# Kernel optimization log

Hardware: AMD Instinct MI355X
Metric: run time of the kernel (lower is better)

Reference implementation:

```python
import jax, jax.numpy as jnp
import numpy as np

N = 100_000   # atoms
B = 10_000    # building blocks
E = 320_000   # edges (bb <- atom)
D = 256       # embed_dim
H = 8         # heads
HD = D // H   # head_dim = 32
DIST = 64     # gaussian dist embed dim
MAX_R = 10.0


def setup_inputs() -> dict:
    key = jax.random.key(0)
    ks = jax.random.split(key, 10)
    atom_feats = jax.random.normal(ks[0], (N, D), jnp.float32)
    coords = jax.random.normal(ks[1], (N, 3), jnp.float32) * 3.0
    bb_vec = jnp.sort(jax.random.randint(ks[2], (N,), 0, B, jnp.int32))
    src = jax.random.randint(ks[3], (E,), 0, N, jnp.int32)
    tgt = jax.random.randint(ks[4], (E,), 0, B, jnp.int32)
    # linear params, [in, out] layout (x @ W + b)
    Wq = jax.random.normal(ks[5], (D, D), jnp.float32) / np.sqrt(D)
    Wk = jax.random.normal(ks[6], (D + DIST, D), jnp.float32) / np.sqrt(D + DIST)
    Wv = jax.random.normal(ks[7], (D + DIST, D), jnp.float32) / np.sqrt(D + DIST)
    Wo = jax.random.normal(ks[8], (D, D), jnp.float32) / np.sqrt(D)
    bq = jnp.zeros((D,), jnp.float32)
    bk = jnp.zeros((D,), jnp.float32)
    bv = jnp.zeros((D,), jnp.float32)
    bo = jnp.zeros((D,), jnp.float32)
    return dict(atom_feats=atom_feats, coords=coords, Wq=Wq, bq=bq, Wk=Wk, bk=bk,
                Wv=Wv, bv=bv, Wo=Wo, bo=bo, bb_vec=bb_vec, src=src, tgt=tgt)


def _gaussian_smearing(dist):
    offsets = jnp.linspace(0.0, MAX_R, DIST)            # [DIST]
    coeff = -0.5 / (offsets[1] - offsets[0]) ** 2
    return jnp.exp(coeff * (dist[:, None] - offsets) ** 2)  # [E, DIST]


def reference(atom_feats, coords, Wq, bq, Wk, bk, Wv, bv, Wo, bo, bb_vec, src, tgt):
    # building-block centers: mean coords, summed feats per bb
    counts = jax.ops.segment_sum(jnp.ones((N,), coords.dtype), bb_vec, num_segments=B)
    bb_center_pos = jax.ops.segment_sum(coords, bb_vec, num_segments=B)
    bb_center_pos = bb_center_pos / jnp.maximum(counts, 1.0)[:, None]       # [B, 3]
    bb_center_feats = jax.ops.segment_sum(atom_feats, bb_vec, num_segments=B)  # [B, D]

    # per-edge distance embedding
    edge_vec = coords[src] - bb_center_pos[tgt]                             # [E, 3]
    dist = jnp.sqrt(jnp.sum(edge_vec * edge_vec, axis=-1))                  # [E]
    edge_dist_embed = _gaussian_smearing(dist)                              # [E, DIST]

    # QKV
    q = (bb_center_feats @ Wq + bq).reshape(B, H, HD)                       # [B, H, HD]
    atom_input = jnp.concatenate([atom_feats[src], edge_dist_embed], -1)    # [E, D+DIST]
    k = (atom_input @ Wk + bk).reshape(E, H, HD)
    v = (atom_input @ Wv + bv).reshape(E, H, HD)

    # per-edge attention logits + segment softmax over tgt
    attn = jnp.einsum('ehc,ehc->eh', q[tgt], k) / np.sqrt(HD)               # [E, H]
    seg_max = jax.ops.segment_max(attn, tgt, num_segments=B)                # [B, H]
    ex = jnp.exp(attn - seg_max[tgt])
    denom = jax.ops.segment_sum(ex, tgt, num_segments=B)                    # [B, H]
    attn = ex / (denom[tgt] + 1e-16)

    # weighted scatter-sum of messages
    msg = attn[..., None] * v                                               # [E, H, HD]
    out = jax.ops.segment_sum(msg, tgt, num_segments=B).reshape(B, D)       # [B, D]
    return out @ Wo + bo
```

## Files before the change

### kernel.cpp

```cpp
#include <hip/hip_runtime.h>
#include <math.h>

#define N_ATOMS 100000
#define B_BB    10000
#define E_EDGES 320000
#define D_DIM   256
#define NHEAD   8
#define NDIST   64
#define EPAD    128

#define DELTA   (10.0f/63.0f)
#define GCOEFF  (-0.5f/(DELTA*DELTA))
#define QKSCALE 0.17677669529663687f

__global__ void k_offsets(const int* __restrict__ bb_vec, int* __restrict__ atom_off,
                          int* __restrict__ edge_cnt) {
  int b = blockIdx.x * 256 + threadIdx.x;
  if (b <= B_BB) {
    int lo = 0, hi = N_ATOMS;
    while (lo < hi) { int mid = (lo + hi) >> 1; if (bb_vec[mid] < b) lo = mid + 1; else hi = mid; }
    atom_off[b] = lo;
  }
  if (b < B_BB) edge_cnt[b] = 0;
}

__global__ __launch_bounds__(256) void k_bb_centers(
    const float* __restrict__ af, const float* __restrict__ coords,
    const int* __restrict__ atom_off, float* __restrict__ bbF, float* __restrict__ bb_pos) {
  int t = threadIdx.x;
  for (int b = blockIdx.x; b < B_BB; b += gridDim.x) {
    int s = atom_off[b], e = atom_off[b + 1];
    float acc = 0.f;
    for (int a = s; a < e; a++) acc += af[(size_t)a * D_DIM + t];
    bbF[(size_t)b * D_DIM + t] = acc;
    if (t < 3) {
      float c = 0.f;
      for (int a = s; a < e; a++) c += coords[(size_t)a * 3 + t];
      float cnt = (float)(e - s);
      bb_pos[b * 4 + t] = c / fmaxf(cnt, 1.0f);
    }
  }
}

__global__ __launch_bounds__(256) void k_gemm256(
    const float* __restrict__ A, const float* __restrict__ W,
    const float* __restrict__ bias, float* __restrict__ C, int M) {
  __shared__ __align__(16) float As[16][68];
  __shared__ __align__(16) float Ws[16][64];
  int tid = threadIdx.x;
  int tx = tid & 15, ty = tid >> 4;
  int row0 = blockIdx.x * 64, col0 = blockIdx.y * 64;
  float acc[4][4] = {};
  for (int k0 = 0; k0 < 256; k0 += 16) {
    {
      int r = tid >> 2;
      int c = (tid & 3) * 4;
      int row = row0 + r;
      float4 v = make_float4(0.f, 0.f, 0.f, 0.f);
      if (row < M) v = *(const float4*)&A[(size_t)row * 256 + k0 + c];
      As[c + 0][r] = v.x; As[c + 1][r] = v.y; As[c + 2][r] = v.z; As[c + 3][r] = v.w;
    }
    {
      int r = tid >> 4;
      int c = (tid & 15) * 4;
      float4 v = *(const float4*)&W[(size_t)(k0 + r) * 256 + col0 + c];
      *(float4*)&Ws[r][c] = v;
    }
    __syncthreads();
#pragma unroll
    for (int kk = 0; kk < 16; kk++) {
      float4 a = *(const float4*)&As[kk][ty * 4];
      float4 b = *(const float4*)&Ws[kk][tx * 4];
      float av[4] = {a.x, a.y, a.z, a.w};
      float bv4[4] = {b.x, b.y, b.z, b.w};
#pragma unroll
      for (int i = 0; i < 4; i++)
#pragma unroll
        for (int j = 0; j < 4; j++) acc[i][j] += av[i] * bv4[j];
    }
    __syncthreads();
  }
#pragma unroll
  for (int i = 0; i < 4; i++) {
    int row = row0 + ty * 4 + i;
    if (row < M) {
      int col = col0 + tx * 4;
      float4 r = make_float4(acc[i][0] + bias[col + 0], acc[i][1] + bias[col + 1],
                             acc[i][2] + bias[col + 2], acc[i][3] + bias[col + 3]);
      *(float4*)&C[(size_t)row * 256 + col] = r;
    }
  }
}

__global__ void k_hist(const int* __restrict__ tgt, int* __restrict__ edge_cnt) {
  int e = blockIdx.x * 256 + threadIdx.x;
  if (e < E_EDGES) atomicAdd(&edge_cnt[tgt[e]], 1);
}

__global__ __launch_bounds__(1024) void k_scan(
    const int* __restrict__ edge_cnt, int* __restrict__ edge_start, int* __restrict__ cursor,
    int* __restrict__ src_sorted, float* __restrict__ dist_sorted) {
  __shared__ int ssum[1024];
  int tid = threadIdx.x;
  int base = tid * 10;
  int v[10]; int s = 0;
#pragma unroll
  for (int k = 0; k < 10; k++) { int i = base + k; v[k] = (i < B_BB) ? edge_cnt[i] : 0; s += v[k]; }
  ssum[tid] = s;
  __syncthreads();
  for (int off = 1; off < 1024; off <<= 1) {
    int t = (tid >= off) ? ssum[tid - off] : 0;
    __syncthreads();
    ssum[tid] += t;
    __syncthreads();
  }
  int excl = ssum[tid] - s;
#pragma unroll
  for (int k = 0; k < 10; k++) {
    int i = base + k;
    if (i < B_BB) { edge_start[i] = excl; cursor[i] = excl; }
    excl += v[k];
  }
  if (tid == 1023) edge_start[B_BB] = E_EDGES;
  if (tid < EPAD) { src_sorted[E_EDGES + tid] = 0; dist_sorted[E_EDGES + tid] = 0.f; }
}

__global__ void k_fill(const int* __restrict__ src, const int* __restrict__ tgt,
                       const float* __restrict__ coords, const float* __restrict__ bb_pos,
                       int* __restrict__ cursor, int* __restrict__ src_sorted,
                       float* __restrict__ dist_sorted) {
  int e = blockIdx.x * 256 + threadIdx.x;
  if (e >= E_EDGES) return;
  int b = tgt[e], a = src[e];
  int pos = atomicAdd(&cursor[b], 1);
  float dx = coords[a * 3 + 0] - bb_pos[b * 4 + 0];
  float dy = coords[a * 3 + 1] - bb_pos[b * 4 + 1];
  float dz = coords[a * 3 + 2] - bb_pos[b * 4 + 2];
  src_sorted[pos] = a;
  dist_sorted[pos] = sqrtf(dx * dx + dy * dy + dz * dz);
}

__global__ __launch_bounds__(256) void k_wt(
    const float* __restrict__ q, const float* __restrict__ Wk, float* __restrict__ wt) {
  __shared__ __align__(16) float As[32][132];
  __shared__ __align__(16) float Bs[32][68];
  int tid = threadIdx.x;
  int b0 = blockIdx.x * 128;
  int i0 = blockIdx.y * 64;
  int h  = blockIdx.z;
  {
    int r = tid >> 1, c0 = (tid & 1) * 16;
    int row = b0 + r;
    const float* qp = q + (size_t)row * 256 + h * 32 + c0;
#pragma unroll
    for (int jj = 0; jj < 4; ++jj) {
      float4 v = make_float4(0.f, 0.f, 0.f, 0.f);
      if (row < B_BB) v = *(const float4*)(qp + 4 * jj);
      As[c0 + 4*jj + 0][r] = v.x; As[c0 + 4*jj + 1][r] = v.y;
      As[c0 + 4*jj + 2][r] = v.z; As[c0 + 4*jj + 3][r] = v.w;
    }
  }
  {
    int r = tid >> 2, c0 = (tid & 3) * 8;
    const float* wp = Wk + (size_t)(i0 + r) * 256 + h * 32 + c0;
#pragma unroll
    for (int jj = 0; jj < 2; ++jj) {
      float4 v = *(const float4*)(wp + 4 * jj);
      Bs[c0 + 4*jj + 0][r] = v.x; Bs[c0 + 4*jj + 1][r] = v.y;
      Bs[c0 + 4*jj + 2][r] = v.z; Bs[c0 + 4*jj + 3][r] = v.w;
    }
  }
  __syncthreads();
  int tx = tid & 15, ty = tid >> 4;
  float acc[8][4] = {};
#pragma unroll
  for (int kk = 0; kk < 32; ++kk) {
    float4 a0 = *(const float4*)&As[kk][ty * 8];
    float4 a1 = *(const float4*)&As[kk][ty * 8 + 4];
    float4 b4 = *(const float4*)&Bs[kk][tx * 4];
    float av[8] = {a0.x, a0.y, a0.z, a0.w, a1.x, a1.y, a1.z, a1.w};
    float bv4[4] = {b4.x, b4.y, b4.z, b4.w};
#pragma unroll
    for (int i = 0; i < 8; ++i)
#pragma unroll
      for (int j = 0; j < 4; ++j) acc[i][j] += av[i] * bv4[j];
  }
#pragma unroll
  for (int i = 0; i < 8; ++i) {
    int row = b0 + ty * 8 + i;
    if (row < B_BB) {
      float4 o = make_float4(acc[i][0] * QKSCALE, acc[i][1] * QKSCALE,
                             acc[i][2] * QKSCALE, acc[i][3] * QKSCALE);
      *(float4*)&wt[(size_t)row * 2560 + h * 320 + i0 + tx * 4] = o;
    }
  }
}

#define FMA4(p, v, Wb, k) \
  p = fmaf((v).x, Wb[(k)], p);   p = fmaf((v).y, Wb[(k)+1], p); \
  p = fmaf((v).z, Wb[(k)+2], p); p = fmaf((v).w, Wb[(k)+3], p);

#define ACC4(Sarr, k, ww, v) \
  Sarr[(k)]   = fmaf(ww, (v).x, Sarr[(k)]);   Sarr[(k)+1] = fmaf(ww, (v).y, Sarr[(k)+1]); \
  Sarr[(k)+2] = fmaf(ww, (v).z, Sarr[(k)+2]); Sarr[(k)+3] = fmaf(ww, (v).w, Sarr[(k)+3]);

__global__ __launch_bounds__(256) void k_attn(
    const float* __restrict__ af, float* __restrict__ wtS,
    const int* __restrict__ edge_start, const int* __restrict__ src_sorted,
    const float* __restrict__ dist_sorted, float* __restrict__ wsum) {
  int tid = threadIdx.x;
  int lane = tid & 63;
  int wv = tid >> 6;
  int h0 = 2 * wv, h1 = 2 * wv + 1;
  int g = lane >> 4;
  int sub = lane & 15;
  int b = blockIdx.x;

  int s0 = edge_start[b], e1 = edge_start[b + 1];
  float* wtb = wtS + (size_t)b * 2560;
  const float* wr0 = wtb + h0 * 320;
  const float* wr1 = wtb + h1 * 320;

  float W0[16], W1[16], wd0[4], wd1[4];
#pragma unroll
  for (int j = 0; j < 4; ++j) {
    float4 t0 = *(const float4*)(wr0 + sub * 16 + 4 * j);
    float4 t1 = *(const float4*)(wr1 + sub * 16 + 4 * j);
    W0[4*j+0] = t0.x; W0[4*j+1] = t0.y; W0[4*j+2] = t0.z; W0[4*j+3] = t0.w;
    W1[4*j+0] = t1.x; W1[4*j+1] = t1.y; W1[4*j+2] = t1.z; W1[4*j+3] = t1.w;
  }
#pragma unroll
  for (int j = 0; j < 4; ++j) { wd0[j] = wr0[256 + sub + 16*j]; wd1[j] = wr1[256 + sub + 16*j]; }

  float cj[4];
#pragma unroll
  for (int j = 0; j < 4; ++j) cj[j] = (float)(sub + 16 * j) * DELTA;

  float l0 = 0.f, l1 = 0.f;
  float S0r[16] = {}, S1r[16] = {};
  float sd0[4] = {}, sd1[4] = {};

  if (s0 < e1) {
    int aC = src_sorted[s0 + g];
    float dC = dist_sorted[s0 + g];
    int aN = src_sorted[s0 + 4 + g];
    float dN = dist_sorted[s0 + 4 + g];
    const float4* crow = (const float4*)(af + (size_t)aC * 256 + sub * 16);
    float4 A0 = crow[0], A1 = crow[1], A2 = crow[2], A3 = crow[3];

    for (int cb = s0; cb < e1; cb += 16) {
      float w0r[4], w1r[4];
      int   a0r[4];
#pragma unroll
      for (int it = 0; it < 4; ++it) {
        int eb = cb + 4 * it;
        const float4* nrow = (const float4*)(af + (size_t)aN * 256 + sub * 16);
        float4 P0 = nrow[0], P1 = nrow[1], P2 = nrow[2], P3 = nrow[3];
        int i2 = eb + 8 + g;
        int aN2 = src_sorted[i2];
        float dN2 = dist_sorted[i2];

        float emb[4];
#pragma unroll
        for (int j = 0; j < 4; ++j) {
          float dd = dC - cj[j];
          emb[j] = __expf(GCOEFF * dd * dd);
        }
        float p0 = 0.f, p1 = 0.f;
        FMA4(p0, A0, W0, 0);  FMA4(p1, A0, W1, 0);
        FMA4(p0, A1, W0, 4);  FMA4(p1, A1, W1, 4);
        FMA4(p0, A2, W0, 8);  FMA4(p1, A2, W1, 8);
        FMA4(p0, A3, W0, 12); FMA4(p1, A3, W1, 12);
#pragma unroll
        for (int j = 0; j < 4; ++j) { p0 = fmaf(emb[j], wd0[j], p0); p1 = fmaf(emb[j], wd1[j], p1); }
#pragma unroll
        for (int off = 8; off > 0; off >>= 1) {
          p0 += __shfl_xor(p0, off);
          p1 += __shfl_xor(p1, off);
        }
        float w0 = __expf(p0), w1 = __expf(p1);
        if (eb + g >= e1) { w0 = 0.f; w1 = 0.f; }
        l0 += w0; l1 += w1;
#pragma unroll
        for (int j = 0; j < 4; ++j) {
          sd0[j] = fmaf(w0, emb[j], sd0[j]);
          sd1[j] = fmaf(w1, emb[j], sd1[j]);
        }
        w0r[it] = w0; w1r[it] = w1; a0r[it] = aC;
        A0 = P0; A1 = P1; A2 = P2; A3 = P3;
        aC = aN; dC = dN;
        aN = aN2; dN = dN2;
      }
#pragma unroll
      for (int it = 0; it < 4; ++it) {
        const float4* rrow = (const float4*)(af + (size_t)a0r[it] * 256 + sub * 16);
        float4 R0 = rrow[0], R1 = rrow[1], R2 = rrow[2], R3 = rrow[3];
        float w0 = w0r[it], w1 = w1r[it];
        ACC4(S0r, 0,  w0, R0); ACC4(S1r, 0,  w1, R0);
        ACC4(S0r, 4,  w0, R1); ACC4(S1r, 4,  w1, R1);
        ACC4(S0r, 8,  w0, R2); ACC4(S1r, 8,  w1, R2);
        ACC4(S0r, 12, w0, R3); ACC4(S1r, 12, w1, R3);
      }
    }
  }

#pragma unroll
  for (int off = 16; off <= 32; off <<= 1) {
    l0 += __shfl_xor(l0, off);
    l1 += __shfl_xor(l1, off);
#pragma unroll
    for (int c = 0; c < 16; ++c) {
      S0r[c] += __shfl_xor(S0r[c], off);
      S1r[c] += __shfl_xor(S1r[c], off);
    }
#pragma unroll
    for (int j = 0; j < 4; ++j) {
      sd0[j] += __shfl_xor(sd0[j], off);
      sd1[j] += __shfl_xor(sd1[j], off);
    }
  }

  float inv0 = 1.0f / (l0 + 1e-16f), inv1 = 1.0f / (l1 + 1e-16f);
  if (g == 0) {
#pragma unroll
    for (int j = 0; j < 4; ++j) {
      float4 o0 = make_float4(S0r[4*j+0]*inv0, S0r[4*j+1]*inv0, S0r[4*j+2]*inv0, S0r[4*j+3]*inv0);
      float4 o1 = make_float4(S1r[4*j+0]*inv1, S1r[4*j+1]*inv1, S1r[4*j+2]*inv1, S1r[4*j+3]*inv1);
      *(float4*)(wtb + h0 * 320 + sub * 16 + 4 * j) = o0;
      *(float4*)(wtb + h1 * 320 + sub * 16 + 4 * j) = o1;
    }
#pragma unroll
    for (int j = 0; j < 4; ++j) {
      wtb[h0 * 320 + 256 + sub + 16 * j] = sd0[j] * inv0;
      wtb[h1 * 320 + 256 + sub + 16 * j] = sd1[j] * inv1;
    }
    if (sub == 0) {
      wsum[b * 8 + h0] = l0 * inv0;
      wsum[b * 8 + h1] = l1 * inv1;
    }
  }
}

__global__ __launch_bounds__(256) void k_out_head(
    const float* __restrict__ Sf, const float* __restrict__ Wv,
    const float* __restrict__ bv, const float* __restrict__ wsum,
    float* __restrict__ out_pre) {
  __shared__ __align__(16) float As[32][132];
  __shared__ __align__(16) float Bs[32][36];
  int tid = threadIdx.x;
  int b0 = blockIdx.x * 128;
  int h  = blockIdx.y;
  int tx = tid & 7, ty = tid >> 3;
  float acc[4][4] = {};
  for (int k0 = 0; k0 < 320; k0 += 32) {
    {
      int r = tid >> 1, c0 = (tid & 1) * 16;
      int row = b0 + r;
      const float* sp = Sf + (size_t)row * 2560 + h * 320 + k0 + c0;
#pragma unroll
      for (int jj = 0; jj < 4; ++jj) {
        float4 v = make_float4(0.f, 0.f, 0.f, 0.f);
        if (row < B_BB) v = *(const float4*)(sp + 4 * jj);
        As[c0 + 4*jj + 0][r] = v.x; As[c0 + 4*jj + 1][r] = v.y;
        As[c0 + 4*jj + 2][r] = v.z; As[c0 + 4*jj + 3][r] = v.w;
      }
    }
    {
      int r = tid >> 3, c0 = (tid & 7) * 4;
      float4 v = *(const float4*)&Wv[(size_t)(k0 + r) * 256 + h * 32 + c0];
      *(float4*)&Bs[r][c0] = v;
    }
    __syncthreads();
#pragma unroll
    for (int kk = 0; kk < 32; ++kk) {
      float4 a4 = *(const float4*)&As[kk][ty * 4];
      float4 b4 = *(const float4*)&Bs[kk][tx * 4];
      float av[4] = {a4.x, a4.y, a4.z, a4.w};
      float bv4[4] = {b4.x, b4.y, b4.z, b4.w};
#pragma unroll
      for (int i = 0; i < 4; ++i)
#pragma unroll
        for (int j = 0; j < 4; ++j) acc[i][j] += av[i] * bv4[j];
    }
    __syncthreads();
  }
  float bvv[4];
#pragma unroll
  for (int j = 0; j < 4; ++j) bvv[j] = bv[h * 32 + tx * 4 + j];
#pragma unroll
  for (int i = 0; i < 4; ++i) {
    int row = b0 + ty * 4 + i;
    if (row < B_BB) {
      float ws = wsum[row * 8 + h];
      float4 o = make_float4(acc[i][0] + ws * bvv[0], acc[i][1] + ws * bvv[1],
                             acc[i][2] + ws * bvv[2], acc[i][3] + ws * bvv[3]);
      *(float4*)&out_pre[(size_t)row * 256 + h * 32 + tx * 4] = o;
    }
  }
}

extern "C" void kernel_launch(void* const* d_in, const int* in_sizes, int n_in,
                              void* d_out, int out_size, void* d_ws, size_t ws_size,
                              hipStream_t stream) {
  const float* af     = (const float*)d_in[0];
  const float* coords = (const float*)d_in[1];
  const float* Wq     = (const float*)d_in[2];
  const float* bq     = (const float*)d_in[3];
  const float* Wk     = (const float*)d_in[4];
  const float* bk     = (const float*)d_in[5];  (void)bk;
  const float* Wv     = (const float*)d_in[6];
  const float* bv     = (const float*)d_in[7];
  const float* Wo     = (const float*)d_in[8];
  const float* bo     = (const float*)d_in[9];
  const int* bb_vec   = (const int*)d_in[10];
  const int* src      = (const int*)d_in[11];
  const int* tgt      = (const int*)d_in[12];
  float* out = (float*)d_out;
  (void)in_sizes; (void)n_in; (void)out_size; (void)ws_size;

  char* ws = (char*)d_ws;
  size_t o = 0;
  auto alloc = [&](size_t bytes) { size_t r = o; o += (bytes + 255) & ~(size_t)255; return r; };
  int*   atom_off    = (int*)(ws + alloc((B_BB + 1) * 4));
  int*   edge_cnt    = (int*)(ws + alloc((size_t)B_BB * 4));
  int*   edge_start  = (int*)(ws + alloc((B_BB + 1) * 4));
  int*   cursor      = (int*)(ws + alloc((size_t)B_BB * 4));
  int*   src_sorted  = (int*)(ws + alloc((size_t)(E_EDGES + EPAD) * 4));
  float* dist_sorted = (float*)(ws + alloc((size_t)(E_EDGES + EPAD) * 4));
  float* bbF         = (float*)(ws + alloc((size_t)B_BB * 256 * 4));
  float* bb_pos      = (float*)(ws + alloc((size_t)B_BB * 4 * 4));
  float* q           = (float*)(ws + alloc((size_t)B_BB * 256 * 4));
  float* wtS         = (float*)(ws + alloc((size_t)B_BB * 2560 * 4));
  float* wsum        = (float*)(ws + alloc((size_t)B_BB * 8 * 4));
  float* out_pre     = (float*)(ws + alloc((size_t)B_BB * 256 * 4));

  k_offsets<<<(B_BB + 1 + 255) / 256, 256, 0, stream>>>(bb_vec, atom_off, edge_cnt);
  k_bb_centers<<<2560, 256, 0, stream>>>(af, coords, atom_off, bbF, bb_pos);
  k_hist<<<(E_EDGES + 255) / 256, 256, 0, stream>>>(tgt, edge_cnt);
  k_scan<<<1, 1024, 0, stream>>>(edge_cnt, edge_start, cursor, src_sorted, dist_sorted);
  k_fill<<<(E_EDGES + 255) / 256, 256, 0, stream>>>(src, tgt, coords, bb_pos, cursor,
                                                    src_sorted, dist_sorted);
  k_gemm256<<<dim3((B_BB + 63) / 64, 4), 256, 0, stream>>>(bbF, Wq, bq, q, B_BB);
  k_wt<<<dim3((B_BB + 127) / 128, 5, 8), 256, 0, stream>>>(q, Wk, wtS);
  k_attn<<<B_BB, 256, 0, stream>>>(af, wtS, edge_start, src_sorted, dist_sorted, wsum);
  k_out_head<<<dim3((B_BB + 127) / 128, 8), 256, 0, stream>>>(wtS, Wv, bv, wsum, out_pre);
  k_gemm256<<<dim3((B_BB + 63) / 64, 4), 256, 0, stream>>>(out_pre, Wo, bo, out, B_BB);
}
```

Before: 642.8 us.

## Keep gathered atom rows in registers for attention accumulation; enlarge GEMM tiles

The attention kernel used to load each gathered atom-feature row twice, once for the logit dot product and again for the weighted sum. It now streams rows through a three-deep register pipeline and reuses the same registers for the accumulation, which halves gather traffic. This costs more live registers per thread. Separately, the dense GEMM tile grows from 64x64 with K-step 16 to 128x64 with K-step 32, raising reuse per thread at the cost of more registers and fewer blocks.

```diff
diff --git a/kernel.cpp b/kernel.cpp
--- a/kernel.cpp
+++ b/kernel.cpp
@@ -45,44 +45,51 @@
 __global__ __launch_bounds__(256) void k_gemm256(
     const float* __restrict__ A, const float* __restrict__ W,
     const float* __restrict__ bias, float* __restrict__ C, int M) {
-  __shared__ __align__(16) float As[16][68];
-  __shared__ __align__(16) float Ws[16][64];
+  __shared__ __align__(16) float As[32][132];
+  __shared__ __align__(16) float Ws[32][68];
   int tid = threadIdx.x;
   int tx = tid & 15, ty = tid >> 4;
-  int row0 = blockIdx.x * 64, col0 = blockIdx.y * 64;
-  float acc[4][4] = {};
-  for (int k0 = 0; k0 < 256; k0 += 16) {
+  int row0 = blockIdx.x * 128, col0 = blockIdx.y * 64;
+  float acc[8][4] = {};
+  for (int k0 = 0; k0 < 256; k0 += 32) {
     {
-      int r = tid >> 2;
-      int c = (tid & 3) * 4;
+      int r = tid >> 1, c0 = (tid & 1) * 16;
       int row = row0 + r;
-      float4 v = make_float4(0.f, 0.f, 0.f, 0.f);
-      if (row < M) v = *(const float4*)&A[(size_t)row * 256 + k0 + c];
-      As[c + 0][r] = v.x; As[c + 1][r] = v.y; As[c + 2][r] = v.z; As[c + 3][r] = v.w;
+      const float* ap = A + (size_t)row * 256 + k0 + c0;
+#pragma unroll
+      for (int jj = 0; jj < 4; ++jj) {
+        float4 v = make_float4(0.f, 0.f, 0.f, 0.f);
+        if (row < M) v = *(const float4*)(ap + 4 * jj);
+        As[c0 + 4*jj + 0][r] = v.x; As[c0 + 4*jj + 1][r] = v.y;
+        As[c0 + 4*jj + 2][r] = v.z; As[c0 + 4*jj + 3][r] = v.w;
+      }
     }
     {
-      int r = tid >> 4;
-      int c = (tid & 15) * 4;
-      float4 v = *(const float4*)&W[(size_t)(k0 + r) * 256 + col0 + c];
-      *(float4*)&Ws[r][c] = v;
-    }
-    __syncthreads();
-#pragma unroll
-    for (int kk = 0; kk < 16; kk++) {
-      float4 a = *(const float4*)&As[kk][ty * 4];
-      float4 b = *(const float4*)&Ws[kk][tx * 4];
-      float av[4] = {a.x, a.y, a.z, a.w};
-      float bv4[4] = {b.x, b.y, b.z, b.w};
-#pragma unroll
-      for (int i = 0; i < 4; i++)
-#pragma unroll
-        for (int j = 0; j < 4; j++) acc[i][j] += av[i] * bv4[j];
-    }
-    __syncthreads();
-  }
-#pragma unroll
-  for (int i = 0; i < 4; i++) {
-    int row = row0 + ty * 4 + i;
+      int r = tid >> 3, c0 = (tid & 7) * 8;
+      const float* wp = W + (size_t)(k0 + r) * 256 + col0 + c0;
+      float4 v0 = *(const float4*)(wp);
+      float4 v1 = *(const float4*)(wp + 4);
+      *(float4*)&Ws[r][c0] = v0;
+      *(float4*)&Ws[r][c0 + 4] = v1;
+    }
+    __syncthreads();
+#pragma unroll
+    for (int kk = 0; kk < 32; ++kk) {
+      float4 a0 = *(const float4*)&As[kk][ty * 8];
+      float4 a1 = *(const float4*)&As[kk][ty * 8 + 4];
+      float4 b4 = *(const float4*)&Ws[kk][tx * 4];
+      float av[8] = {a0.x, a0.y, a0.z, a0.w, a1.x, a1.y, a1.z, a1.w};
+      float bv4[4] = {b4.x, b4.y, b4.z, b4.w};
+#pragma unroll
+      for (int i = 0; i < 8; ++i)
+#pragma unroll
+        for (int j = 0; j < 4; ++j) acc[i][j] += av[i] * bv4[j];
+    }
+    __syncthreads();
+  }
+#pragma unroll
+  for (int i = 0; i < 8; ++i) {
+    int row = row0 + ty * 8 + i;
     if (row < M) {
       int col = col0 + tx * 4;
       float4 r = make_float4(acc[i][0] + bias[col + 0], acc[i][1] + bias[col + 1],
@@ -241,66 +248,58 @@
   float sd0[4] = {}, sd1[4] = {};
 
   if (s0 < e1) {
-    int aC = src_sorted[s0 + g];
-    float dC = dist_sorted[s0 + g];
-    int aN = src_sorted[s0 + 4 + g];
-    float dN = dist_sorted[s0 + 4 + g];
-    const float4* crow = (const float4*)(af + (size_t)aC * 256 + sub * 16);
-    float4 A0 = crow[0], A1 = crow[1], A2 = crow[2], A3 = crow[3];
-
-    for (int cb = s0; cb < e1; cb += 16) {
-      float w0r[4], w1r[4];
-      int   a0r[4];
-#pragma unroll
-      for (int it = 0; it < 4; ++it) {
-        int eb = cb + 4 * it;
-        const float4* nrow = (const float4*)(af + (size_t)aN * 256 + sub * 16);
-        float4 P0 = nrow[0], P1 = nrow[1], P2 = nrow[2], P3 = nrow[3];
-        int i2 = eb + 8 + g;
-        int aN2 = src_sorted[i2];
-        float dN2 = dist_sorted[i2];
-
-        float emb[4];
-#pragma unroll
-        for (int j = 0; j < 4; ++j) {
-          float dd = dC - cj[j];
-          emb[j] = __expf(GCOEFF * dd * dd);
-        }
-        float p0 = 0.f, p1 = 0.f;
-        FMA4(p0, A0, W0, 0);  FMA4(p1, A0, W1, 0);
-        FMA4(p0, A1, W0, 4);  FMA4(p1, A1, W1, 4);
-        FMA4(p0, A2, W0, 8);  FMA4(p1, A2, W1, 8);
-        FMA4(p0, A3, W0, 12); FMA4(p1, A3, W1, 12);
-#pragma unroll
-        for (int j = 0; j < 4; ++j) { p0 = fmaf(emb[j], wd0[j], p0); p1 = fmaf(emb[j], wd1[j], p1); }
-#pragma unroll
-        for (int off = 8; off > 0; off >>= 1) {
-          p0 += __shfl_xor(p0, off);
-          p1 += __shfl_xor(p1, off);
-        }
-        float w0 = __expf(p0), w1 = __expf(p1);
-        if (eb + g >= e1) { w0 = 0.f; w1 = 0.f; }
-        l0 += w0; l1 += w1;
-#pragma unroll
-        for (int j = 0; j < 4; ++j) {
-          sd0[j] = fmaf(w0, emb[j], sd0[j]);
-          sd1[j] = fmaf(w1, emb[j], sd1[j]);
-        }
-        w0r[it] = w0; w1r[it] = w1; a0r[it] = aC;
-        A0 = P0; A1 = P1; A2 = P2; A3 = P3;
-        aC = aN; dC = dN;
-        aN = aN2; dN = dN2;
+    int ia0 = src_sorted[s0 + g];
+    int ia1 = src_sorted[s0 + 4 + g];
+    int ia2 = src_sorted[s0 + 8 + g];
+    float dd0 = dist_sorted[s0 + g];
+    float dd1 = dist_sorted[s0 + 4 + g];
+    float dd2 = dist_sorted[s0 + 8 + g];
+    const float4* r0p = (const float4*)(af + (size_t)ia0 * 256 + sub * 16);
+    const float4* r1p = (const float4*)(af + (size_t)ia1 * 256 + sub * 16);
+    float4 A0 = r0p[0], A1 = r0p[1], A2 = r0p[2], A3 = r0p[3];
+    float4 B0 = r1p[0], B1 = r1p[1], B2 = r1p[2], B3 = r1p[3];
+
+    for (int eb = s0; eb < e1; eb += 4) {
+      const float4* r2p = (const float4*)(af + (size_t)ia2 * 256 + sub * 16);
+      float4 C0 = r2p[0], C1 = r2p[1], C2 = r2p[2], C3 = r2p[3];
+      int ia3 = src_sorted[eb + 12 + g];
+      float dd3 = dist_sorted[eb + 12 + g];
+
+      float emb[4];
+#pragma unroll
+      for (int j = 0; j < 4; ++j) {
+        float dd = dd0 - cj[j];
+        emb[j] = __expf(GCOEFF * dd * dd);
       }
-#pragma unroll
-      for (int it = 0; it < 4; ++it) {
-        const float4* rrow = (const float4*)(af + (size_t)a0r[it] * 256 + sub * 16);
-        float4 R0 = rrow[0], R1 = rrow[1], R2 = rrow[2], R3 = rrow[3];
-        float w0 = w0r[it], w1 = w1r[it];
-        ACC4(S0r, 0,  w0, R0); ACC4(S1r, 0,  w1, R0);
-        ACC4(S0r, 4,  w0, R1); ACC4(S1r, 4,  w1, R1);
-        ACC4(S0r, 8,  w0, R2); ACC4(S1r, 8,  w1, R2);
-        ACC4(S0r, 12, w0, R3); ACC4(S1r, 12, w1, R3);
+      float p0 = 0.f, p1 = 0.f;
+      FMA4(p0, A0, W0, 0);  FMA4(p1, A0, W1, 0);
+      FMA4(p0, A1, W0, 4);  FMA4(p1, A1, W1, 4);
+      FMA4(p0, A2, W0, 8);  FMA4(p1, A2, W1, 8);
+      FMA4(p0, A3, W0, 12); FMA4(p1, A3, W1, 12);
+#pragma unroll
+      for (int j = 0; j < 4; ++j) { p0 = fmaf(emb[j], wd0[j], p0); p1 = fmaf(emb[j], wd1[j], p1); }
+#pragma unroll
+      for (int off = 8; off > 0; off >>= 1) {
+        p0 += __shfl_xor(p0, off);
+        p1 += __shfl_xor(p1, off);
       }
+      float w0 = __expf(p0), w1 = __expf(p1);
+      if (eb + g >= e1) { w0 = 0.f; w1 = 0.f; }
+      l0 += w0; l1 += w1;
+      ACC4(S0r, 0,  w0, A0); ACC4(S1r, 0,  w1, A0);
+      ACC4(S0r, 4,  w0, A1); ACC4(S1r, 4,  w1, A1);
+      ACC4(S0r, 8,  w0, A2); ACC4(S1r, 8,  w1, A2);
+      ACC4(S0r, 12, w0, A3); ACC4(S1r, 12, w1, A3);
+#pragma unroll
+      for (int j = 0; j < 4; ++j) {
+        sd0[j] = fmaf(w0, emb[j], sd0[j]);
+        sd1[j] = fmaf(w1, emb[j], sd1[j]);
+      }
+
+      A0 = B0; A1 = B1; A2 = B2; A3 = B3;
+      B0 = C0; B1 = C1; B2 = C2; B3 = C3;
+      dd0 = dd1; dd1 = dd2; dd2 = dd3;
+      ia2 = ia3;
     }
   }
 
@@ -440,9 +439,9 @@
   k_scan<<<1, 1024, 0, stream>>>(edge_cnt, edge_start, cursor, src_sorted, dist_sorted);
   k_fill<<<(E_EDGES + 255) / 256, 256, 0, stream>>>(src, tgt, coords, bb_pos, cursor,
                                                     src_sorted, dist_sorted);
-  k_gemm256<<<dim3((B_BB + 63) / 64, 4), 256, 0, stream>>>(bbF, Wq, bq, q, B_BB);
+  k_gemm256<<<dim3((B_BB + 127) / 128, 4), 256, 0, stream>>>(bbF, Wq, bq, q, B_BB);
   k_wt<<<dim3((B_BB + 127) / 128, 5, 8), 256, 0, stream>>>(q, Wk, wtS);
   k_attn<<<B_BB, 256, 0, stream>>>(af, wtS, edge_start, src_sorted, dist_sorted, wsum);
   k_out_head<<<dim3((B_BB + 127) / 128, 8), 256, 0, stream>>>(wtS, Wv, bv, wsum, out_pre);
-  k_gemm256<<<dim3((B_BB + 63) / 64, 4), 256, 0, stream>>>(out_pre, Wo, bo, out, B_BB);
-}
+  k_gemm256<<<dim3((B_BB + 127) / 128, 4), 256, 0, stream>>>(out_pre, Wo, bo, out, B_BB);
+}
```

New measurement: 567.3 us. 11.8% less time.

## Stage gathered atom rows in double-buffered LDS shared across waves

Applied to the files above, without the earlier changes.

Each of the four waves used to gather the same atom feature rows from global memory on its own, and read each row twice (once for the logit, once for the weighted sum). Now the block cooperatively loads 8 edge rows per step into a double-buffered LDS tile, and every wave reads from that shared copy. Each row is therefore fetched from global memory once per block, and the value accumulation reuses the registers already loaded for the logit. The cost is a __syncthreads per 8 edges, about 16KB of LDS, and possible LDS bank conflicts from the strided float4 reads.

```diff
diff --git a/kernel.cpp b/kernel.cpp
--- a/kernel.cpp
+++ b/kernel.cpp
@@ -208,12 +208,15 @@
     const float* __restrict__ af, float* __restrict__ wtS,
     const int* __restrict__ edge_start, const int* __restrict__ src_sorted,
     const float* __restrict__ dist_sorted, float* __restrict__ wsum) {
+  __shared__ __align__(16) float4 lbuf[2][8][65];
   int tid = threadIdx.x;
   int lane = tid & 63;
   int wv = tid >> 6;
   int h0 = 2 * wv, h1 = 2 * wv + 1;
   int g = lane >> 4;
   int sub = lane & 15;
+  int srow = tid >> 5;
+  int schunk = tid & 31;
   int b = blockIdx.x;
 
   int s0 = edge_start[b], e1 = edge_start[b + 1];
@@ -241,31 +244,30 @@
   float sd0[4] = {}, sd1[4] = {};
 
   if (s0 < e1) {
-    int aC = src_sorted[s0 + g];
-    float dC = dist_sorted[s0 + g];
-    int aN = src_sorted[s0 + 4 + g];
-    float dN = dist_sorted[s0 + 4 + g];
-    const float4* crow = (const float4*)(af + (size_t)aC * 256 + sub * 16);
-    float4 A0 = crow[0], A1 = crow[1], A2 = crow[2], A3 = crow[3];
-
-    for (int cb = s0; cb < e1; cb += 16) {
-      float w0r[4], w1r[4];
-      int   a0r[4];
-#pragma unroll
-      for (int it = 0; it < 4; ++it) {
-        int eb = cb + 4 * it;
-        const float4* nrow = (const float4*)(af + (size_t)aN * 256 + sub * 16);
-        float4 P0 = nrow[0], P1 = nrow[1], P2 = nrow[2], P3 = nrow[3];
-        int i2 = eb + 8 + g;
-        int aN2 = src_sorted[i2];
-        float dN2 = dist_sorted[i2];
-
+    {
+      int idx = src_sorted[s0 + srow];
+      const float4* rp = (const float4*)(af + (size_t)idx * 256);
+      lbuf[0][srow][schunk]      = rp[schunk];
+      lbuf[0][srow][schunk + 32] = rp[schunk + 32];
+    }
+    __syncthreads();
+    int cur = 0;
+
+    for (int eb = s0; eb < e1; eb += 8) {
+      int nidx = src_sorted[eb + 8 + srow];
+      const float4* np = (const float4*)(af + (size_t)nidx * 256);
+      float4 n0 = np[schunk];
+      float4 n1 = np[schunk + 32];
+
+      float dA = dist_sorted[eb + g];
+      float dB = dist_sorted[eb + 4 + g];
+
+      {
+        const float4* row = &lbuf[cur][g][0];
+        float4 A0 = row[sub*4+0], A1 = row[sub*4+1], A2 = row[sub*4+2], A3 = row[sub*4+3];
         float emb[4];
 #pragma unroll
-        for (int j = 0; j < 4; ++j) {
-          float dd = dC - cj[j];
-          emb[j] = __expf(GCOEFF * dd * dd);
-        }
+        for (int j = 0; j < 4; ++j) { float dd = dA - cj[j]; emb[j] = __expf(GCOEFF * dd * dd); }
         float p0 = 0.f, p1 = 0.f;
         FMA4(p0, A0, W0, 0);  FMA4(p1, A0, W1, 0);
         FMA4(p0, A1, W0, 4);  FMA4(p1, A1, W1, 4);
@@ -281,26 +283,52 @@
         float w0 = __expf(p0), w1 = __expf(p1);
         if (eb + g >= e1) { w0 = 0.f; w1 = 0.f; }
         l0 += w0; l1 += w1;
+        ACC4(S0r, 0,  w0, A0); ACC4(S1r, 0,  w1, A0);
+        ACC4(S0r, 4,  w0, A1); ACC4(S1r, 4,  w1, A1);
+        ACC4(S0r, 8,  w0, A2); ACC4(S1r, 8,  w1, A2);
+        ACC4(S0r, 12, w0, A3); ACC4(S1r, 12, w1, A3);
 #pragma unroll
         for (int j = 0; j < 4; ++j) {
           sd0[j] = fmaf(w0, emb[j], sd0[j]);
           sd1[j] = fmaf(w1, emb[j], sd1[j]);
         }
-        w0r[it] = w0; w1r[it] = w1; a0r[it] = aC;
-        A0 = P0; A1 = P1; A2 = P2; A3 = P3;
-        aC = aN; dC = dN;
-        aN = aN2; dN = dN2;
       }
-#pragma unroll
-      for (int it = 0; it < 4; ++it) {
-        const float4* rrow = (const float4*)(af + (size_t)a0r[it] * 256 + sub * 16);
-        float4 R0 = rrow[0], R1 = rrow[1], R2 = rrow[2], R3 = rrow[3];
-        float w0 = w0r[it], w1 = w1r[it];
-        ACC4(S0r, 0,  w0, R0); ACC4(S1r, 0,  w1, R0);
-        ACC4(S0r, 4,  w0, R1); ACC4(S1r, 4,  w1, R1);
-        ACC4(S0r, 8,  w0, R2); ACC4(S1r, 8,  w1, R2);
-        ACC4(S0r, 12, w0, R3); ACC4(S1r, 12, w1, R3);
+      {
+        const float4* row = &lbuf[cur][4 + g][0];
+        float4 A0 = row[sub*4+0], A1 = row[sub*4+1], A2 = row[sub*4+2], A3 = row[sub*4+3];
+        float emb[4];
+#pragma unroll
+        for (int j = 0; j < 4; ++j) { float dd = dB - cj[j]; emb[j] = __expf(GCOEFF * dd * dd); }
+        float p0 = 0.f, p1 = 0.f;
+        FMA4(p0, A0, W0, 0);  FMA4(p1, A0, W1, 0);
+        FMA4(p0, A1, W0, 4);  FMA4(p1, A1, W1, 4);
+        FMA4(p0, A2, W0, 8);  FMA4(p1, A2, W1, 8);
+        FMA4(p0, A3, W0, 12); FMA4(p1, A3, W1, 12);
+#pragma unroll
+        for (int j = 0; j < 4; ++j) { p0 = fmaf(emb[j], wd0[j], p0); p1 = fmaf(emb[j], wd1[j], p1); }
+#pragma unroll
+        for (int off = 8; off > 0; off >>= 1) {
+          p0 += __shfl_xor(p0, off);
+          p1 += __shfl_xor(p1, off);
+        }
+        float w0 = __expf(p0), w1 = __expf(p1);
+        if (eb + 4 + g >= e1) { w0 = 0.f; w1 = 0.f; }
+        l0 += w0; l1 += w1;
+        ACC4(S0r, 0,  w0, A0); ACC4(S1r, 0,  w1, A0);
+        ACC4(S0r, 4,  w0, A1); ACC4(S1r, 4,  w1, A1);
+        ACC4(S0r, 8,  w0, A2); ACC4(S1r, 8,  w1, A2);
+        ACC4(S0r, 12, w0, A3); ACC4(S1r, 12, w1, A3);
+#pragma unroll
+        for (int j = 0; j < 4; ++j) {
+          sd0[j] = fmaf(w0, emb[j], sd0[j]);
+          sd1[j] = fmaf(w1, emb[j], sd1[j]);
+        }
       }
+
+      lbuf[cur ^ 1][srow][schunk]      = n0;
+      lbuf[cur ^ 1][srow][schunk + 32] = n1;
+      __syncthreads();
+      cur ^= 1;
     }
   }
 
```

After: 597.1 us. -7.1%, faster.

## Reuse gathered atom rows for value accumulation and double-buffer two edges

Applied to the files above, without the earlier changes.

The edge loop now processes two edge groups per iteration and keeps each gathered atom-feature row in registers for both the logit dot product and the weighted value accumulation. Before, every row was fetched a second time for the accumulation pass. Rows are prefetched two groups ahead, with the loads for the next pair issued between compute phases to hide gather latency. This removes the duplicate global/L2 row reads and adds instruction-level parallelism, at the cost of more live registers, which could lower occupancy.

```diff
diff --git a/kernel.cpp b/kernel.cpp
--- a/kernel.cpp
+++ b/kernel.cpp
@@ -241,66 +241,82 @@
   float sd0[4] = {}, sd1[4] = {};
 
   if (s0 < e1) {
-    int aC = src_sorted[s0 + g];
-    float dC = dist_sorted[s0 + g];
-    int aN = src_sorted[s0 + 4 + g];
-    float dN = dist_sorted[s0 + 4 + g];
-    const float4* crow = (const float4*)(af + (size_t)aC * 256 + sub * 16);
-    float4 A0 = crow[0], A1 = crow[1], A2 = crow[2], A3 = crow[3];
-
-    for (int cb = s0; cb < e1; cb += 16) {
-      float w0r[4], w1r[4];
-      int   a0r[4];
-#pragma unroll
-      for (int it = 0; it < 4; ++it) {
-        int eb = cb + 4 * it;
-        const float4* nrow = (const float4*)(af + (size_t)aN * 256 + sub * 16);
-        float4 P0 = nrow[0], P1 = nrow[1], P2 = nrow[2], P3 = nrow[3];
-        int i2 = eb + 8 + g;
-        int aN2 = src_sorted[i2];
-        float dN2 = dist_sorted[i2];
-
-        float emb[4];
-#pragma unroll
-        for (int j = 0; j < 4; ++j) {
-          float dd = dC - cj[j];
-          emb[j] = __expf(GCOEFF * dd * dd);
-        }
-        float p0 = 0.f, p1 = 0.f;
-        FMA4(p0, A0, W0, 0);  FMA4(p1, A0, W1, 0);
-        FMA4(p0, A1, W0, 4);  FMA4(p1, A1, W1, 4);
-        FMA4(p0, A2, W0, 8);  FMA4(p1, A2, W1, 8);
-        FMA4(p0, A3, W0, 12); FMA4(p1, A3, W1, 12);
-#pragma unroll
-        for (int j = 0; j < 4; ++j) { p0 = fmaf(emb[j], wd0[j], p0); p1 = fmaf(emb[j], wd1[j], p1); }
-#pragma unroll
-        for (int off = 8; off > 0; off >>= 1) {
-          p0 += __shfl_xor(p0, off);
-          p1 += __shfl_xor(p1, off);
-        }
-        float w0 = __expf(p0), w1 = __expf(p1);
-        if (eb + g >= e1) { w0 = 0.f; w1 = 0.f; }
-        l0 += w0; l1 += w1;
-#pragma unroll
-        for (int j = 0; j < 4; ++j) {
-          sd0[j] = fmaf(w0, emb[j], sd0[j]);
-          sd1[j] = fmaf(w1, emb[j], sd1[j]);
-        }
-        w0r[it] = w0; w1r[it] = w1; a0r[it] = aC;
-        A0 = P0; A1 = P1; A2 = P2; A3 = P3;
-        aC = aN; dC = dN;
-        aN = aN2; dN = dN2;
+    int iaC = src_sorted[s0 + 8 + g];
+    int iaD = src_sorted[s0 + 12 + g];
+    float ddA = dist_sorted[s0 + g];
+    float ddB = dist_sorted[s0 + 4 + g];
+    float ddC = dist_sorted[s0 + 8 + g];
+    float ddD = dist_sorted[s0 + 12 + g];
+    int iaA = src_sorted[s0 + g];
+    int iaB = src_sorted[s0 + 4 + g];
+    const float4* rA = (const float4*)(af + (size_t)iaA * 256 + sub * 16);
+    const float4* rB = (const float4*)(af + (size_t)iaB * 256 + sub * 16);
+    float4 A0 = rA[0], A1 = rA[1], A2 = rA[2], A3 = rA[3];
+    float4 B0 = rB[0], B1 = rB[1], B2 = rB[2], B3 = rB[3];
+
+    for (int eb = s0; eb < e1; eb += 8) {
+      int iaC2 = src_sorted[eb + 16 + g];
+      float ddC2 = dist_sorted[eb + 16 + g];
+      int iaD2 = src_sorted[eb + 20 + g];
+      float ddD2 = dist_sorted[eb + 20 + g];
+      const float4* rC = (const float4*)(af + (size_t)iaC * 256 + sub * 16);
+      float4 C0 = rC[0], C1 = rC[1], C2 = rC[2], C3 = rC[3];
+
+      float embA[4], embB[4];
+#pragma unroll
+      for (int j = 0; j < 4; ++j) {
+        float da = ddA - cj[j]; embA[j] = __expf(GCOEFF * da * da);
+        float db = ddB - cj[j]; embB[j] = __expf(GCOEFF * db * db);
       }
-#pragma unroll
-      for (int it = 0; it < 4; ++it) {
-        const float4* rrow = (const float4*)(af + (size_t)a0r[it] * 256 + sub * 16);
-        float4 R0 = rrow[0], R1 = rrow[1], R2 = rrow[2], R3 = rrow[3];
-        float w0 = w0r[it], w1 = w1r[it];
-        ACC4(S0r, 0,  w0, R0); ACC4(S1r, 0,  w1, R0);
-        ACC4(S0r, 4,  w0, R1); ACC4(S1r, 4,  w1, R1);
-        ACC4(S0r, 8,  w0, R2); ACC4(S1r, 8,  w1, R2);
-        ACC4(S0r, 12, w0, R3); ACC4(S1r, 12, w1, R3);
+      float pA0 = 0.f, pA1 = 0.f, pB0 = 0.f, pB1 = 0.f;
+      FMA4(pA0, A0, W0, 0);  FMA4(pA1, A0, W1, 0);
+      FMA4(pB0, B0, W0, 0);  FMA4(pB1, B0, W1, 0);
+      FMA4(pA0, A1, W0, 4);  FMA4(pA1, A1, W1, 4);
+      FMA4(pB0, B1, W0, 4);  FMA4(pB1, B1, W1, 4);
+      FMA4(pA0, A2, W0, 8);  FMA4(pA1, A2, W1, 8);
+      FMA4(pB0, B2, W0, 8);  FMA4(pB1, B2, W1, 8);
+      FMA4(pA0, A3, W0, 12); FMA4(pA1, A3, W1, 12);
+      FMA4(pB0, B3, W0, 12); FMA4(pB1, B3, W1, 12);
+#pragma unroll
+      for (int j = 0; j < 4; ++j) {
+        pA0 = fmaf(embA[j], wd0[j], pA0); pA1 = fmaf(embA[j], wd1[j], pA1);
+        pB0 = fmaf(embB[j], wd0[j], pB0); pB1 = fmaf(embB[j], wd1[j], pB1);
       }
+#pragma unroll
+      for (int off = 8; off > 0; off >>= 1) {
+        pA0 += __shfl_xor(pA0, off);
+        pA1 += __shfl_xor(pA1, off);
+        pB0 += __shfl_xor(pB0, off);
+        pB1 += __shfl_xor(pB1, off);
+      }
+      float wA0 = __expf(pA0), wA1 = __expf(pA1);
+      float wB0 = __expf(pB0), wB1 = __expf(pB1);
+      if (eb + g >= e1)     { wA0 = 0.f; wA1 = 0.f; }
+      if (eb + 4 + g >= e1) { wB0 = 0.f; wB1 = 0.f; }
+      l0 += wA0 + wB0; l1 += wA1 + wB1;
+#pragma unroll
+      for (int j = 0; j < 4; ++j) {
+        sd0[j] = fmaf(wA0, embA[j], sd0[j]); sd1[j] = fmaf(wA1, embA[j], sd1[j]);
+        sd0[j] = fmaf(wB0, embB[j], sd0[j]); sd1[j] = fmaf(wB1, embB[j], sd1[j]);
+      }
+
+      ACC4(S0r, 0,  wA0, A0); ACC4(S1r, 0,  wA1, A0);
+      ACC4(S0r, 4,  wA0, A1); ACC4(S1r, 4,  wA1, A1);
+      ACC4(S0r, 8,  wA0, A2); ACC4(S1r, 8,  wA1, A2);
+      ACC4(S0r, 12, wA0, A3); ACC4(S1r, 12, wA1, A3);
+
+      const float4* rD = (const float4*)(af + (size_t)iaD * 256 + sub * 16);
+      float4 D0 = rD[0], D1 = rD[1], D2 = rD[2], D3 = rD[3];
+
+      ACC4(S0r, 0,  wB0, B0); ACC4(S1r, 0,  wB1, B0);
+      ACC4(S0r, 4,  wB0, B1); ACC4(S1r, 4,  wB1, B1);
+      ACC4(S0r, 8,  wB0, B2); ACC4(S1r, 8,  wB1, B2);
+      ACC4(S0r, 12, wB0, B3); ACC4(S1r, 12, wB1, B3);
+
+      A0 = C0; A1 = C1; A2 = C2; A3 = C3;
+      B0 = D0; B1 = D1; B2 = D2; B3 = D3;
+      ddA = ddC; ddB = ddD; ddC = ddC2; ddD = ddD2;
+      iaC = iaC2; iaD = iaD2;
     }
   }
 
```

Measured after the change: 557.7 us. 13.3% less time.
